# Kernel optimization log

Hardware: AMD Instinct MI355X
Metric: run time of the kernel (lower is better)

Reference implementation:

```python
import jax, jax.numpy as jnp
import numpy as np

N_HEAD, D_MODEL, D_HEAD, D_OUT = 16, 1024, 64, 1024
Q_INNER = N_HEAD * D_HEAD


def setup_inputs() -> dict:
    key = jax.random.key(0)
    ks = jax.random.split(key, 10)
    B, S = 1, 4096
    hidden_state = jax.random.normal(ks[0], (B, S, D_MODEL), dtype=jnp.float32)
    # causal mask, (B,1,S,S), 1 = attend, 0 = masked
    attention_mask = jnp.tril(jnp.ones((S, S), dtype=jnp.int32))[None, None, :, :]
    s = 0.02
    Wq = jax.random.normal(ks[1], (D_MODEL, Q_INNER), dtype=jnp.float32) * s
    bq = jnp.zeros((Q_INNER,), dtype=jnp.float32)
    Wk = jax.random.normal(ks[2], (D_MODEL, D_HEAD), dtype=jnp.float32) * s
    bk = jnp.zeros((D_HEAD,), dtype=jnp.float32)
    Wv = jax.random.normal(ks[3], (D_MODEL, D_HEAD), dtype=jnp.float32) * s
    bv = jnp.zeros((D_HEAD,), dtype=jnp.float32)
    Wo = jax.random.normal(ks[4], (Q_INNER, D_OUT), dtype=jnp.float32) * s
    bo = jnp.zeros((D_OUT,), dtype=jnp.float32)
    return {"hidden_state": hidden_state, "attention_mask": attention_mask,
            "Wq": Wq, "bq": bq, "Wk": Wk, "bk": bk, "Wv": Wv, "bv": bv,
            "Wo": Wo, "bo": bo}


def reference(hidden_state, attention_mask, Wq, bq, Wk, bk, Wv, bv, Wo, bo):
    B, S, _ = hidden_state.shape
    q = hidden_state @ Wq + bq                    # (B,S,H*Dh)
    k = hidden_state @ Wk + bk                    # (B,S,Dh) single shared KV head
    v = hidden_state @ Wv + bv                    # (B,S,Dh)
    q = q.reshape(B, S, N_HEAD, D_HEAD)           # (B,S,H,Dh)
    scale = 1.0 / jnp.sqrt(jnp.float32(D_HEAD))
    # scores: (B,H,S,S) — shared K broadcast over heads
    scores = jnp.einsum('bqhd,bkd->bhqk', q, k) * scale
    scores = jnp.where(attention_mask == 0, -jnp.inf, scores)
    probs = jax.nn.softmax(scores, axis=-1)
    out = jnp.einsum('bhqk,bkd->bqhd', probs, v)  # (B,S,H,Dh)
    out = out.reshape(B, S, Q_INNER)
    return out @ Wo + bo
```

## Files before the change

### kernel.cpp

```cpp
#include <hip/hip_runtime.h>
#include <hip/hip_bf16.h>
#include <math.h>

typedef __bf16 bf16;
typedef __bf16 bf16x4 __attribute__((ext_vector_type(4)));
typedef __bf16 bf16x8 __attribute__((ext_vector_type(8)));
typedef float f32x4 __attribute__((ext_vector_type(4)));

#define AS1(p) ((const __attribute__((address_space(1))) void*)(p))
#define AS3(p) ((__attribute__((address_space(3))) void*)(p))

__device__ __forceinline__ void gld_lds16(const void* g, void* l) {
  __builtin_amdgcn_global_load_lds(AS1(g), AS3(l), 16, 0, 0);
}

#define MFMA16(a, b, c) __builtin_amdgcn_mfma_f32_16x16x32_bf16((a), (b), (c), 0, 0, 0)

#define QSCALE_F 0.180336880f


struct Seg { short qt, h, t0, t1, slot; };
struct Tape { Seg s[1008]; };
struct CJob { short qt, h, base, parts; };
struct CTab { CJob j[336]; };

constexpr int nparts_of(int qt) { int T = 2 * qt + 2; return (T + 21) / 22; }
constexpr int slot_base(int h, int qt) {
  int b = h * 52;
  if (qt <= 21) return b + (qt - 11) * 2;
  return b + 22 + (qt - 22) * 3;
}

constexpr Tape make_tape() {
  Tape tp{};
  int idx = 0;
  for (int s = 22; s >= 1; --s)
    for (int h = 0; h < 16; ++h)
      for (int qt = 0; qt < 32; ++qt) {
        const int T = 2 * qt + 2, P = nparts_of(qt);
        for (int p = 0; p < P; ++p) {
          const int a = p * T / P, b = (p + 1) * T / P;
          if (b - a == s) {
            const int slot = (P == 1) ? -1 : slot_base(h, qt) + p;
            tp.s[idx++] = Seg{(short)qt, (short)h, (short)a, (short)b, (short)slot};
          }
        }
      }
  return tp;
}

constexpr CTab make_ctab() {
  CTab ct{};
  int n = 0;
  for (int h = 0; h < 16; ++h)
    for (int qt = 11; qt < 32; ++qt)
      ct.j[n++] = CJob{(short)qt, (short)h, (short)slot_base(h, qt),
                       (short)nparts_of(qt)};
  return ct;
}

__device__ constexpr Tape TAPE = make_tape();
__device__ constexpr CTab CTAB = make_ctab();

__global__ void cast_f32_bf16_sw(const float4* __restrict__ in, bf16* __restrict__ out,
                                 int n4) {
  int i = blockIdx.x * blockDim.x + threadIdx.x;
  if (i < n4) {
    float4 v = in[i];
    bf16x4 o4 = {(bf16)v.x, (bf16)v.y, (bf16)v.z, (bf16)v.w};
    const int e = i * 4;
    const int row = e >> 10;
    const int idx = (e & ~63) | ((e & 63) ^ ((row & 7) << 3));
    *(bf16x4*)(out + (size_t)idx) = o4;
  }
}

__global__ void prep_wqkv(const float* __restrict__ Wq, const float* __restrict__ Wk,
                          const float* __restrict__ Wv, bf16* __restrict__ out) {
  __shared__ float t[64][65];
  const int ob = blockIdx.y;
  const float* src;
  int C, c0;
  if (ob < 16)      { src = Wq; C = 1024; c0 = ob * 64; }
  else if (ob == 16){ src = Wk; C = 64;   c0 = 0; }
  else              { src = Wv; C = 64;   c0 = 0; }
  const int r0 = blockIdx.x * 64;
  const int tx = threadIdx.x & 63, ty = threadIdx.x >> 6;
#pragma unroll
  for (int j = 0; j < 16; j++)
    t[ty + j * 4][tx] = src[(size_t)(r0 + ty + j * 4) * C + c0 + tx];
  __syncthreads();
#pragma unroll
  for (int j = 0; j < 16; j++) {
    const int orow = ob * 64 + ty + j * 4;
    out[(size_t)orow * 1024 + r0 + (tx ^ ((orow & 7) << 3))] = (bf16)t[tx][ty + j * 4];
  }
}

__global__ void transpose_cast_sw(const float* __restrict__ in, bf16* __restrict__ out,
                                  int C, int ldout) {
  __shared__ float t[64][65];
  int r0 = blockIdx.y * 64, c0 = blockIdx.x * 64;
  int tx = threadIdx.x & 63, ty = threadIdx.x >> 6;
#pragma unroll
  for (int j = 0; j < 16; j++)
    t[ty + j * 4][tx] = in[(size_t)(r0 + ty + j * 4) * C + c0 + tx];
  __syncthreads();
#pragma unroll
  for (int j = 0; j < 16; j++) {
    const int orow = c0 + ty + j * 4;
    out[(size_t)orow * ldout + r0 + (tx ^ ((orow & 7) << 3))] = (bf16)t[tx][ty + j * 4];
  }
}

__global__ void pack_bias3(const float* __restrict__ bq, const float* __restrict__ bk,
                           const float* __restrict__ bv, float* __restrict__ o) {
  int i = blockIdx.x * 256 + threadIdx.x;
  if (i < 1024) o[i] = bq[i];
  else if (i < 1088) o[i] = bk[i - 1024];
  else if (i < 1152) o[i] = bv[i - 1088];
}

template <int OUTF32, int QSCALE>
__global__ __launch_bounds__(256) void gemm_bt64k(const bf16* __restrict__ A,
                                                  const bf16* __restrict__ B,
                                                  const float* __restrict__ bias,
                                                  void* __restrict__ Cout,
                                                  int M, int N, int K) {
  __shared__ bf16 As[2 * 64 * 64];
  __shared__ bf16 Bs[2 * 128 * 64];
  const int tid = threadIdx.x, w = tid >> 6, lane = tid & 63;
  const int g = lane >> 4, r = lane & 15;
  const int cpx = gridDim.x >> 3;
  const int l = (blockIdx.x & 7) * cpx + (blockIdx.x >> 3);
  const int ntn = N >> 7;
  const int my = l / ntn, mx = l - my * ntn;
  const int tm = my * 64, tn = mx * 128;
  const int wr = w >> 1, wc = w & 1;
  const int sz = (r & 7) << 4;

  f32x4 acc[2][4] = {};

  const char* gA = (const char*)(A + (size_t)tm * K);
  const char* gB = (const char*)(B + (size_t)tn * K);
  const int linA0 = (w * 2 + 0) * 1024 + lane * 16;
  const int linA1 = (w * 2 + 1) * 1024 + lane * 16;
  const int linB0 = (w * 4 + 0) * 1024 + lane * 16;
  const int linB1 = (w * 4 + 1) * 1024 + lane * 16;
  const int linB2 = (w * 4 + 2) * 1024 + lane * 16;
  const int linB3 = (w * 4 + 3) * 1024 + lane * 16;

  auto STAGE = [&](int ks, int b) {
    char* dA = (char*)As + b * 8192 + (w * 2) * 1024;
    char* dB = (char*)Bs + b * 16384 + (w * 4) * 1024;
    gld_lds16(gA + (size_t)(linA0 >> 7) * (K * 2) + ks * 128 + (linA0 & 127), dA);
    gld_lds16(gA + (size_t)(linA1 >> 7) * (K * 2) + ks * 128 + (linA1 & 127), dA + 1024);
    gld_lds16(gB + (size_t)(linB0 >> 7) * (K * 2) + ks * 128 + (linB0 & 127), dB);
    gld_lds16(gB + (size_t)(linB1 >> 7) * (K * 2) + ks * 128 + (linB1 & 127), dB + 1024);
    gld_lds16(gB + (size_t)(linB2 >> 7) * (K * 2) + ks * 128 + (linB2 & 127), dB + 2048);
    gld_lds16(gB + (size_t)(linB3 >> 7) * (K * 2) + ks * 128 + (linB3 & 127), dB + 3072);
  };

  const int nk = K >> 6;
  STAGE(0, 0);
  int buf = 0;
  for (int ks = 0; ks < nk; ++ks) {
    if (ks + 1 < nk) {
      STAGE(ks + 1, buf ^ 1);
      asm volatile("s_waitcnt vmcnt(6)" ::: "memory");
    } else {
      asm volatile("s_waitcnt vmcnt(0)" ::: "memory");
    }
    __builtin_amdgcn_sched_barrier(0);
    __builtin_amdgcn_s_barrier();

    const char* at = (const char*)As + buf * 8192;
    const char* bt = (const char*)Bs + buf * 16384;
    bf16x8 af[2][2], bfr[4][2];
#pragma unroll
    for (int m = 0; m < 2; m++)
#pragma unroll
      for (int kk = 0; kk < 2; kk++)
        af[m][kk] = *(const bf16x8*)(at + (wr * 32 + m * 16 + r) * 128 +
                                     ((kk * 64 + g * 16) ^ sz));
#pragma unroll
    for (int n = 0; n < 4; n++)
#pragma unroll
      for (int kk = 0; kk < 2; kk++)
        bfr[n][kk] = *(const bf16x8*)(bt + (wc * 64 + n * 16 + r) * 128 +
                                      ((kk * 64 + g * 16) ^ sz));
    __builtin_amdgcn_s_setprio(1);
#pragma unroll
    for (int m = 0; m < 2; m++)
#pragma unroll
      for (int n = 0; n < 4; n++) {
        acc[m][n] = MFMA16(af[m][0], bfr[n][0], acc[m][n]);
        acc[m][n] = MFMA16(af[m][1], bfr[n][1], acc[m][n]);
      }
    __builtin_amdgcn_s_setprio(0);
    __builtin_amdgcn_s_barrier();
    buf ^= 1;
  }

#pragma unroll
  for (int m = 0; m < 2; m++) {
#pragma unroll
    for (int n = 0; n < 4; n++) {
      int crow = tm + wr * 32 + m * 16 + g * 4;
      int ccol = tn + wc * 64 + n * 16 + r;
      float bb = bias[ccol];
      float sc = (QSCALE && ccol < 1024) ? QSCALE_F : 1.0f;
#pragma unroll
      for (int j = 0; j < 4; j++) {
        float v = (acc[m][n][j] + bb) * sc;
        if (OUTF32)
          ((float*)Cout)[(size_t)(crow + j) * N + ccol] = v;
        else
          ((bf16*)Cout)[(size_t)(crow + j) * N + ccol] = (bf16)v;
      }
    }
  }
}

__global__ void kv_prep(const bf16* __restrict__ QKV, bf16* __restrict__ Ksw,
                        bf16* __restrict__ Vtsw) {
  __shared__ bf16 Vld[64][72];
  const int kv0 = blockIdx.x * 64;
  const int tid = threadIdx.x;
#pragma unroll
  for (int cc = 0; cc < 2; cc++) {
    const int c = tid + cc * 256;
    const int kvl = c >> 3, c8 = c & 7;
    bf16x8 kv8 = *(const bf16x8*)(QKV + (size_t)(kv0 + kvl) * 1152 + 1024 + c8 * 8);
    *(bf16x8*)(Ksw + (size_t)(kv0 + kvl) * 64 + ((c8 * 8) ^ ((kvl & 7) << 3))) = kv8;
    bf16x8 vv = *(const bf16x8*)(QKV + (size_t)(kv0 + kvl) * 1152 + 1088 + c8 * 8);
#pragma unroll
    for (int e = 0; e < 8; e++) Vld[c8 * 8 + e][kvl] = vv[e];
  }
  __syncthreads();
#pragma unroll
  for (int cc = 0; cc < 2; cc++) {
    const int c = tid + cc * 256;
    const int d = c >> 3, k8 = c & 7;
    bf16x8 o8 = *(const bf16x8*)&Vld[d][k8 * 8];
    *(bf16x8*)(Vtsw + (size_t)d * 4096 + kv0 + ((k8 * 8) ^ ((d & 7) << 3))) = o8;
  }
}

__global__ __launch_bounds__(256) void mqa_fwd(const bf16* __restrict__ QKV,
                                               const bf16* __restrict__ Ksw,
                                               const bf16* __restrict__ Vtsw,
                                               bf16* __restrict__ AO,
                                               bf16* __restrict__ po,
                                               float* __restrict__ psum) {
  __shared__ bf16 Ks[2][64 * 64];
  __shared__ bf16 Vs[2][64 * 64];
  __shared__ bf16 Ps[4 * 32 * 64];

  const Seg sg = TAPE.s[blockIdx.x];
  const int qt = sg.qt, h = sg.h, tbeg = sg.t0, tend = sg.t1, slot = sg.slot;

  const int tid = threadIdx.x, w = tid >> 6, lane = tid & 63;
  const int g = lane >> 4, r = lane & 15;
  const int qw = qt * 128 + w * 32;
  const int qown0 = qw + r;
  const int qown1 = qw + 16 + r;

  const char* Kg = (const char*)Ksw;
  const char* Vg = (const char*)Vtsw;
  char* PsB = (char*)Ps;
  const int lin0 = w * 2048 + lane * 16;
  const int lin1 = lin0 + 1024;
  const int sz = (r & 7) << 4;

  bf16x8 qf0[2], qf1[2];
#pragma unroll
  for (int kk = 0; kk < 2; kk++) {
    qf0[kk] = *(const bf16x8*)&QKV[(size_t)qown0 * 1152 + h * 64 + kk * 32 + g * 8];
    qf1[kk] = *(const bf16x8*)&QKV[(size_t)qown1 * 1152 + h * 64 + kk * 32 + g * 8];
  }

  const bf16 one = (bf16)1.0f;
  const bf16x8 ones = {one, one, one, one, one, one, one, one};

  f32x4 o[2][4] = {};
  f32x4 sums[2] = {};

  auto STAGE = [&](int t, int b) {
    const int kn = t * 64;
    char* kb = (char*)Ks + b * 8192 + w * 2048;
    char* vb = (char*)Vs + b * 8192 + w * 2048;
    gld_lds16(Kg + (size_t)kn * 128 + lin0, kb);
    gld_lds16(Kg + (size_t)kn * 128 + lin1, kb + 1024);
    gld_lds16(Vg + (size_t)(lin0 >> 7) * 8192 + kn * 2 + (lin0 & 127), vb);
    gld_lds16(Vg + (size_t)(lin1 >> 7) * 8192 + kn * 2 + (lin1 & 127), vb + 1024);
  };

  int buf = 0;
  STAGE(tbeg, 0);
  for (int t = tbeg; t < tend; ++t) {
    if (t + 1 < tend) {
      STAGE(t + 1, buf ^ 1);
      asm volatile("s_waitcnt vmcnt(4)" ::: "memory");
    } else {
      asm volatile("s_waitcnt vmcnt(0)" ::: "memory");
    }
    __builtin_amdgcn_sched_barrier(0);
    __builtin_amdgcn_s_barrier();

    const char* kt = (const char*)Ks + buf * 8192;
    const char* vt = (const char*)Vs + buf * 8192;
    const int kv0 = t * 64;

    f32x4 s0[4], s1[4];
    __builtin_amdgcn_s_setprio(1);
#pragma unroll
    for (int n = 0; n < 4; n++) {
      bf16x8 kf0 = *(const bf16x8*)(kt + (n * 16 + r) * 128 + ((g * 16) ^ sz));
      bf16x8 kf1 = *(const bf16x8*)(kt + (n * 16 + r) * 128 + ((64 + g * 16) ^ sz));
      f32x4 z0 = {0.f, 0.f, 0.f, 0.f};
      z0 = MFMA16(kf0, qf0[0], z0);
      z0 = MFMA16(kf1, qf0[1], z0);
      s0[n] = z0;
      f32x4 z1 = {0.f, 0.f, 0.f, 0.f};
      z1 = MFMA16(kf0, qf1[0], z1);
      z1 = MFMA16(kf1, qf1[1], z1);
      s1[n] = z1;
    }
    __builtin_amdgcn_s_setprio(0);

    if (t >= 2 * qt) {
#pragma unroll
      for (int n = 0; n < 4; n++)
#pragma unroll
        for (int jj = 0; jj < 4; jj++) {
          const int kv = kv0 + n * 16 + g * 4 + jj;
          if (kv > qown0) s0[n][jj] = -3.0e38f;
          if (kv > qown1) s1[n][jj] = -3.0e38f;
        }
    }

#pragma unroll
    for (int n = 0; n < 4; n++) {
      bf16x4 pk0, pk1;
#pragma unroll
      for (int jj = 0; jj < 4; jj++) {
        pk0[jj] = (bf16)__builtin_amdgcn_exp2f(s0[n][jj]);
        pk1[jj] = (bf16)__builtin_amdgcn_exp2f(s1[n][jj]);
      }
      *(bf16x4*)(PsB + w * 4096 + r * 128 + ((n * 32 + g * 8) ^ sz)) = pk0;
      *(bf16x4*)(PsB + w * 4096 + (16 + r) * 128 + ((n * 32 + g * 8) ^ sz)) = pk1;
    }

    asm volatile("s_waitcnt lgkmcnt(0)" ::: "memory");
    __builtin_amdgcn_sched_barrier(0);

    bf16x8 pa00 = *(const bf16x8*)(PsB + w * 4096 + r * 128 + ((g * 16) ^ sz));
    bf16x8 pa01 = *(const bf16x8*)(PsB + w * 4096 + r * 128 + ((64 + g * 16) ^ sz));
    bf16x8 pa10 = *(const bf16x8*)(PsB + w * 4096 + (16 + r) * 128 + ((g * 16) ^ sz));
    bf16x8 pa11 = *(const bf16x8*)(PsB + w * 4096 + (16 + r) * 128 + ((64 + g * 16) ^ sz));
    __builtin_amdgcn_s_setprio(1);
    sums[0] = MFMA16(pa00, ones, sums[0]);
    sums[0] = MFMA16(pa01, ones, sums[0]);
    sums[1] = MFMA16(pa10, ones, sums[1]);
    sums[1] = MFMA16(pa11, ones, sums[1]);
#pragma unroll
    for (int n = 0; n < 4; n++) {
      bf16x8 vf0 = *(const bf16x8*)(vt + (n * 16 + r) * 128 + ((g * 16) ^ sz));
      bf16x8 vf1 = *(const bf16x8*)(vt + (n * 16 + r) * 128 + ((64 + g * 16) ^ sz));
      o[0][n] = MFMA16(pa00, vf0, o[0][n]);
      o[0][n] = MFMA16(pa01, vf1, o[0][n]);
      o[1][n] = MFMA16(pa10, vf0, o[1][n]);
      o[1][n] = MFMA16(pa11, vf1, o[1][n]);
    }
    __builtin_amdgcn_s_setprio(0);
    __builtin_amdgcn_s_barrier();
    buf ^= 1;
  }

  if (slot < 0) {
#pragma unroll
    for (int H = 0; H < 2; H++)
#pragma unroll
      for (int jj = 0; jj < 4; jj++) {
        const float inv = 1.f / sums[H][jj];
        const int row = qw + H * 16 + g * 4 + jj;
        const int key = (row & 7) << 3;
#pragma unroll
        for (int n = 0; n < 4; n++)
          AO[(size_t)row * 1024 + h * 64 + ((n * 16 + r) ^ key)] =
              (bf16)(o[H][n][jj] * inv);
      }
  } else {
    bf16* pb = po + (size_t)slot * 8192;
#pragma unroll
    for (int H = 0; H < 2; H++)
#pragma unroll
      for (int jj = 0; jj < 4; jj++) {
        const int row = w * 32 + H * 16 + g * 4 + jj;
#pragma unroll
        for (int n = 0; n < 4; n++)
          pb[row * 64 + n * 16 + r] = (bf16)o[H][n][jj];
        if (r == 0) psum[slot * 128 + row] = sums[H][jj];
      }
  }
}

__global__ __launch_bounds__(256) void combine_split(const bf16* __restrict__ po,
                                                     const float* __restrict__ psum,
                                                     bf16* __restrict__ AO) {
  const CJob cj = CTAB.j[blockIdx.x];
  const int row = threadIdx.x >> 1, c0 = (threadIdx.x & 1) * 32;
  float acc[32] = {};
  float ssum = 0.f;
#pragma unroll 1
  for (int p = 0; p < cj.parts; ++p) {
    const bf16* pb = po + (size_t)(cj.base + p) * 8192 + row * 64 + c0;
    ssum += psum[(cj.base + p) * 128 + row];
#pragma unroll
    for (int v = 0; v < 4; ++v) {
      bf16x8 x = ((const bf16x8*)pb)[v];
#pragma unroll
      for (int e = 0; e < 8; e++) acc[v * 8 + e] += (float)x[e];
    }
  }
  const float inv = 1.f / ssum;
  const int grow = cj.qt * 128 + row;
  const int key = (grow & 7) << 3;
  bf16* dst = AO + (size_t)grow * 1024 + cj.h * 64;
#pragma unroll
  for (int i = 0; i < 8; i++) {
    bf16x4 o4 = {(bf16)(acc[i * 4 + 0] * inv), (bf16)(acc[i * 4 + 1] * inv),
                 (bf16)(acc[i * 4 + 2] * inv), (bf16)(acc[i * 4 + 3] * inv)};
    *(bf16x4*)(dst + ((c0 + i * 4) ^ key)) = o4;
  }
}

extern "C" void kernel_launch(void* const* d_in, const int* in_sizes, int n_in,
                              void* d_out, int out_size, void* d_ws, size_t ws_size,
                              hipStream_t stream) {
  const float* H  = (const float*)d_in[0];
  const float* Wq = (const float*)d_in[2];
  const float* bq = (const float*)d_in[3];
  const float* Wk = (const float*)d_in[4];
  const float* bk = (const float*)d_in[5];
  const float* Wv = (const float*)d_in[6];
  const float* bv = (const float*)d_in[7];
  const float* Wo = (const float*)d_in[8];
  const float* bo = (const float*)d_in[9];
  float* out = (float*)d_out;

  const int S = 4096, DM = 1024;

  char* p = (char*)d_ws;
  bf16* Hb    = (bf16*)(p);
  bf16* QKV   = (bf16*)(p + 8388608);
  bf16* Wqkvt = (bf16*)(p + 17825792);
  bf16* Wot   = (bf16*)(p + 20185088);
  float* bqkv = (float*)(p + 22282240);
  bf16* Ksw   = (bf16*)(p + 22286848);
  bf16* Vtsw  = (bf16*)(p + 22811136);
  bf16* po    = (bf16*)(p + 23335424);
  float* psum = (float*)(p + 36966912);
  bf16* AOb   = Hb;

  cast_f32_bf16_sw<<<(S * DM / 4 + 255) / 256, 256, 0, stream>>>((const float4*)H, Hb,
                                                                 S * DM / 4);
  prep_wqkv<<<dim3(16, 18), 256, 0, stream>>>(Wq, Wk, Wv, Wqkvt);
  transpose_cast_sw<<<dim3(16, 16), 256, 0, stream>>>(Wo, Wot, 1024, 1024);
  pack_bias3<<<5, 256, 0, stream>>>(bq, bk, bv, bqkv);

  gemm_bt64k<0, 1><<<576, 256, 0, stream>>>(Hb, Wqkvt, bqkv, QKV, S, 1152, 1024);

  kv_prep<<<64, 256, 0, stream>>>(QKV, Ksw, Vtsw);

  mqa_fwd<<<1008, 256, 0, stream>>>(QKV, Ksw, Vtsw, AOb, po, psum);
  combine_split<<<336, 256, 0, stream>>>(po, psum, AOb);

  gemm_bt64k<1, 0><<<512, 256, 0, stream>>>(AOb, Wot, bo, out, S, 1024, 1024);
}
```

Baseline: 119.9 us.

## Load K/V fragments directly from global into registers, dropping LDS staging

Removes the double-buffered LDS staging of K and V tiles and the block-wide barriers. Each wave now loads its K and V MFMA fragments straight from global memory into registers, prefetching the next K tile during the softmax. Launch bounds request 3 blocks per CU, since LDS use is now small. In exchange the shared K/V tiles are fetched redundantly by all four waves, which relies on the L2/L1 cache, and V loads are exposed to latency within the same iteration.

New measurement: 173.6 us. 44.7% more time.

```diff
diff --git a/kernel.cpp b/kernel.cpp
--- a/kernel.cpp
+++ b/kernel.cpp
@@ -247,14 +247,12 @@
   }
 }
 
-__global__ __launch_bounds__(256) void mqa_fwd(const bf16* __restrict__ QKV,
-                                               const bf16* __restrict__ Ksw,
-                                               const bf16* __restrict__ Vtsw,
-                                               bf16* __restrict__ AO,
-                                               bf16* __restrict__ po,
-                                               float* __restrict__ psum) {
-  __shared__ bf16 Ks[2][64 * 64];
-  __shared__ bf16 Vs[2][64 * 64];
+__global__ __launch_bounds__(256, 3) void mqa_fwd(const bf16* __restrict__ QKV,
+                                                  const bf16* __restrict__ Ksw,
+                                                  const bf16* __restrict__ Vtsw,
+                                                  bf16* __restrict__ AO,
+                                                  bf16* __restrict__ po,
+                                                  float* __restrict__ psum) {
   __shared__ bf16 Ps[4 * 32 * 64];
 
   const Seg sg = TAPE.s[blockIdx.x];
@@ -269,8 +267,6 @@
   const char* Kg = (const char*)Ksw;
   const char* Vg = (const char*)Vtsw;
   char* PsB = (char*)Ps;
-  const int lin0 = w * 2048 + lane * 16;
-  const int lin1 = lin0 + 1024;
   const int sz = (r & 7) << 4;
 
   bf16x8 qf0[2], qf1[2];
@@ -286,48 +282,42 @@
   f32x4 o[2][4] = {};
   f32x4 sums[2] = {};
 
-  auto STAGE = [&](int t, int b) {
-    const int kn = t * 64;
-    char* kb = (char*)Ks + b * 8192 + w * 2048;
-    char* vb = (char*)Vs + b * 8192 + w * 2048;
-    gld_lds16(Kg + (size_t)kn * 128 + lin0, kb);
-    gld_lds16(Kg + (size_t)kn * 128 + lin1, kb + 1024);
-    gld_lds16(Vg + (size_t)(lin0 >> 7) * 8192 + kn * 2 + (lin0 & 127), vb);
-    gld_lds16(Vg + (size_t)(lin1 >> 7) * 8192 + kn * 2 + (lin1 & 127), vb + 1024);
+  bf16x8 kf[4][2];
+  auto LDK = [&](int t) {
+#pragma unroll
+    for (int n = 0; n < 4; n++)
+#pragma unroll
+      for (int kk = 0; kk < 2; kk++)
+        kf[n][kk] = *(const bf16x8*)(Kg + (size_t)t * 8192 + (n * 16 + r) * 128 +
+                                     ((kk * 64 + g * 16) ^ sz));
   };
 
-  int buf = 0;
-  STAGE(tbeg, 0);
+  LDK(tbeg);
   for (int t = tbeg; t < tend; ++t) {
-    if (t + 1 < tend) {
-      STAGE(t + 1, buf ^ 1);
-      asm volatile("s_waitcnt vmcnt(4)" ::: "memory");
-    } else {
-      asm volatile("s_waitcnt vmcnt(0)" ::: "memory");
-    }
-    __builtin_amdgcn_sched_barrier(0);
-    __builtin_amdgcn_s_barrier();
-
-    const char* kt = (const char*)Ks + buf * 8192;
-    const char* vt = (const char*)Vs + buf * 8192;
     const int kv0 = t * 64;
 
     f32x4 s0[4], s1[4];
     __builtin_amdgcn_s_setprio(1);
 #pragma unroll
     for (int n = 0; n < 4; n++) {
-      bf16x8 kf0 = *(const bf16x8*)(kt + (n * 16 + r) * 128 + ((g * 16) ^ sz));
-      bf16x8 kf1 = *(const bf16x8*)(kt + (n * 16 + r) * 128 + ((64 + g * 16) ^ sz));
       f32x4 z0 = {0.f, 0.f, 0.f, 0.f};
-      z0 = MFMA16(kf0, qf0[0], z0);
-      z0 = MFMA16(kf1, qf0[1], z0);
+      z0 = MFMA16(kf[n][0], qf0[0], z0);
+      z0 = MFMA16(kf[n][1], qf0[1], z0);
       s0[n] = z0;
       f32x4 z1 = {0.f, 0.f, 0.f, 0.f};
-      z1 = MFMA16(kf0, qf1[0], z1);
-      z1 = MFMA16(kf1, qf1[1], z1);
+      z1 = MFMA16(kf[n][0], qf1[0], z1);
+      z1 = MFMA16(kf[n][1], qf1[1], z1);
       s1[n] = z1;
     }
     __builtin_amdgcn_s_setprio(0);
+
+    bf16x8 vf[4][2];
+#pragma unroll
+    for (int n = 0; n < 4; n++)
+#pragma unroll
+      for (int kk = 0; kk < 2; kk++)
+        vf[n][kk] = *(const bf16x8*)(Vg + (size_t)(n * 16 + r) * 8192 + kv0 * 2 +
+                                     ((kk * 64 + g * 16) ^ sz));
 
     if (t >= 2 * qt) {
 #pragma unroll
@@ -351,6 +341,8 @@
       *(bf16x4*)(PsB + w * 4096 + r * 128 + ((n * 32 + g * 8) ^ sz)) = pk0;
       *(bf16x4*)(PsB + w * 4096 + (16 + r) * 128 + ((n * 32 + g * 8) ^ sz)) = pk1;
     }
+
+    if (t + 1 < tend) LDK(t + 1);
 
     asm volatile("s_waitcnt lgkmcnt(0)" ::: "memory");
     __builtin_amdgcn_sched_barrier(0);
@@ -366,16 +358,12 @@
     sums[1] = MFMA16(pa11, ones, sums[1]);
 #pragma unroll
     for (int n = 0; n < 4; n++) {
-      bf16x8 vf0 = *(const bf16x8*)(vt + (n * 16 + r) * 128 + ((g * 16) ^ sz));
-      bf16x8 vf1 = *(const bf16x8*)(vt + (n * 16 + r) * 128 + ((64 + g * 16) ^ sz));
-      o[0][n] = MFMA16(pa00, vf0, o[0][n]);
-      o[0][n] = MFMA16(pa01, vf1, o[0][n]);
-      o[1][n] = MFMA16(pa10, vf0, o[1][n]);
-      o[1][n] = MFMA16(pa11, vf1, o[1][n]);
+      o[0][n] = MFMA16(pa00, vf[n][0], o[0][n]);
+      o[0][n] = MFMA16(pa01, vf[n][1], o[0][n]);
+      o[1][n] = MFMA16(pa10, vf[n][0], o[1][n]);
+      o[1][n] = MFMA16(pa11, vf[n][1], o[1][n]);
     }
     __builtin_amdgcn_s_setprio(0);
-    __builtin_amdgcn_s_barrier();
-    buf ^= 1;
   }
 
   if (slot < 0) {
```

## Keep P in registers via 16x16x16 MFMA and rebalance causal split tape

Applied to the files above, without the earlier changes.

Removes the LDS round-trip for the probability tile by feeding exp2 results directly as A-operands of the 16x16x16 bf16 MFMA, whose register layout matches the QK^T accumulator output. V fragments are now read as 4-element chunks per k-block. The work tape is rebuilt by pairing light and heavy causal query tiles (i, 31-i) into four segments per pair, so the grid is exactly 1024 evenly sized blocks, and launch bounds request 4 blocks per CU. It trades twice as many smaller MFMA instructions for fewer LDS writes, reads and waits, and lower LDS use per block.

New measurement: 135.3 us. 12.8% more time.

```diff
diff --git a/kernel.cpp b/kernel.cpp
--- a/kernel.cpp
+++ b/kernel.cpp
@@ -6,6 +6,7 @@
 typedef __bf16 bf16x4 __attribute__((ext_vector_type(4)));
 typedef __bf16 bf16x8 __attribute__((ext_vector_type(8)));
 typedef float f32x4 __attribute__((ext_vector_type(4)));
+typedef short s16x4 __attribute__((ext_vector_type(4)));
 
 #define AS1(p) ((const __attribute__((address_space(1))) void*)(p))
 #define AS3(p) ((__attribute__((address_space(3))) void*)(p))
@@ -15,47 +16,58 @@
 }
 
 #define MFMA16(a, b, c) __builtin_amdgcn_mfma_f32_16x16x32_bf16((a), (b), (c), 0, 0, 0)
+#define MFMA16K(a, b, c) __builtin_amdgcn_mfma_f32_16x16x16bf16_1k((a), (b), (c), 0, 0, 0)
 
 #define QSCALE_F 0.180336880f
 
 
 struct Seg { short qt, h, t0, t1, slot; };
-struct Tape { Seg s[1008]; };
+struct Tape { Seg s[1024]; };
 struct CJob { short qt, h, base, parts; };
 struct CTab { CJob j[336]; };
 
-constexpr int nparts_of(int qt) { int T = 2 * qt + 2; return (T + 21) / 22; }
-constexpr int slot_base(int h, int qt) {
-  int b = h * 52;
-  if (qt <= 21) return b + (qt - 11) * 2;
-  return b + 22 + (qt - 22) * 3;
-}
-
 constexpr Tape make_tape() {
   Tape tp{};
-  int idx = 0;
-  for (int s = 22; s >= 1; --s)
-    for (int h = 0; h < 16; ++h)
-      for (int qt = 0; qt < 32; ++qt) {
-        const int T = 2 * qt + 2, P = nparts_of(qt);
-        for (int p = 0; p < P; ++p) {
-          const int a = p * T / P, b = (p + 1) * T / P;
-          if (b - a == s) {
-            const int slot = (P == 1) ? -1 : slot_base(h, qt) + p;
-            tp.s[idx++] = Seg{(short)qt, (short)h, (short)a, (short)b, (short)slot};
-          }
-        }
-      }
+  int slot_next = 0;
+  for (int h = 0; h < 16; ++h)
+    for (int i = 0; i < 16; ++i) {
+      const int px = h * 16 + i;
+      const int T1 = 2 * i + 2, T2 = 64 - 2 * i;
+      const int a = (T1 <= 22) ? 1 : 2, b = 4 - a;
+      int k = 0;
+      int base1 = -1;
+      if (a > 1) { base1 = slot_next; slot_next += a; }
+      for (int p = 0; p < a; ++p) {
+        const int t0 = p * T1 / a, t1 = (p + 1) * T1 / a;
+        tp.s[px + 256 * k] = Seg{(short)i, (short)h, (short)t0, (short)t1,
+                                 (short)(a > 1 ? base1 + p : -1)};
+        ++k;
+      }
+      const int base2 = slot_next; slot_next += b;
+      for (int p = 0; p < b; ++p) {
+        const int t0 = p * T2 / b, t1 = (p + 1) * T2 / b;
+        tp.s[px + 256 * k] = Seg{(short)(31 - i), (short)h, (short)t0, (short)t1,
+                                 (short)(base2 + p)};
+        ++k;
+      }
+    }
   return tp;
 }
 
 constexpr CTab make_ctab() {
   CTab ct{};
-  int n = 0;
+  int slot_next = 0, nj = 0;
   for (int h = 0; h < 16; ++h)
-    for (int qt = 11; qt < 32; ++qt)
-      ct.j[n++] = CJob{(short)qt, (short)h, (short)slot_base(h, qt),
-                       (short)nparts_of(qt)};
+    for (int i = 0; i < 16; ++i) {
+      const int T1 = 2 * i + 2;
+      const int a = (T1 <= 22) ? 1 : 2, b = 4 - a;
+      if (a > 1) {
+        ct.j[nj++] = CJob{(short)i, (short)h, (short)slot_next, (short)a};
+        slot_next += a;
+      }
+      ct.j[nj++] = CJob{(short)(31 - i), (short)h, (short)slot_next, (short)b};
+      slot_next += b;
+    }
   return ct;
 }
 
@@ -247,15 +259,14 @@
   }
 }
 
-__global__ __launch_bounds__(256) void mqa_fwd(const bf16* __restrict__ QKV,
-                                               const bf16* __restrict__ Ksw,
-                                               const bf16* __restrict__ Vtsw,
-                                               bf16* __restrict__ AO,
-                                               bf16* __restrict__ po,
-                                               float* __restrict__ psum) {
+__global__ __launch_bounds__(256, 4) void mqa_fwd(const bf16* __restrict__ QKV,
+                                                  const bf16* __restrict__ Ksw,
+                                                  const bf16* __restrict__ Vtsw,
+                                                  bf16* __restrict__ AO,
+                                                  bf16* __restrict__ po,
+                                                  float* __restrict__ psum) {
   __shared__ bf16 Ks[2][64 * 64];
   __shared__ bf16 Vs[2][64 * 64];
-  __shared__ bf16 Ps[4 * 32 * 64];
 
   const Seg sg = TAPE.s[blockIdx.x];
   const int qt = sg.qt, h = sg.h, tbeg = sg.t0, tend = sg.t1, slot = sg.slot;
@@ -268,7 +279,6 @@
 
   const char* Kg = (const char*)Ksw;
   const char* Vg = (const char*)Vtsw;
-  char* PsB = (char*)Ps;
   const int lin0 = w * 2048 + lane * 16;
   const int lin1 = lin0 + 1024;
   const int sz = (r & 7) << 4;
@@ -280,11 +290,9 @@
     qf1[kk] = *(const bf16x8*)&QKV[(size_t)qown1 * 1152 + h * 64 + kk * 32 + g * 8];
   }
 
-  const bf16 one = (bf16)1.0f;
-  const bf16x8 ones = {one, one, one, one, one, one, one, one};
-
   f32x4 o[2][4] = {};
   f32x4 sums[2] = {};
+  const s16x4 ones4 = {0x3F80, 0x3F80, 0x3F80, 0x3F80};
 
   auto STAGE = [&](int t, int b) {
     const int kn = t * 64;
@@ -329,6 +337,14 @@
     }
     __builtin_amdgcn_s_setprio(0);
 
+    s16x4 vf[4][4];
+#pragma unroll
+    for (int kb = 0; kb < 4; kb++)
+#pragma unroll
+      for (int n = 0; n < 4; n++)
+        vf[kb][n] = *(const s16x4*)(vt + (n * 16 + r) * 128 +
+                                    ((kb * 32 + g * 8) ^ sz));
+
     if (t >= 2 * qt) {
 #pragma unroll
       for (int n = 0; n < 4; n++)
@@ -340,38 +356,26 @@
         }
     }
 
-#pragma unroll
-    for (int n = 0; n < 4; n++) {
-      bf16x4 pk0, pk1;
+    union PW { bf16x4 hh; s16x4 ss; };
+    PW p0[4], p1[4];
+#pragma unroll
+    for (int n = 0; n < 4; n++)
 #pragma unroll
       for (int jj = 0; jj < 4; jj++) {
-        pk0[jj] = (bf16)__builtin_amdgcn_exp2f(s0[n][jj]);
-        pk1[jj] = (bf16)__builtin_amdgcn_exp2f(s1[n][jj]);
-      }
-      *(bf16x4*)(PsB + w * 4096 + r * 128 + ((n * 32 + g * 8) ^ sz)) = pk0;
-      *(bf16x4*)(PsB + w * 4096 + (16 + r) * 128 + ((n * 32 + g * 8) ^ sz)) = pk1;
-    }
-
-    asm volatile("s_waitcnt lgkmcnt(0)" ::: "memory");
-    __builtin_amdgcn_sched_barrier(0);
-
-    bf16x8 pa00 = *(const bf16x8*)(PsB + w * 4096 + r * 128 + ((g * 16) ^ sz));
-    bf16x8 pa01 = *(const bf16x8*)(PsB + w * 4096 + r * 128 + ((64 + g * 16) ^ sz));
-    bf16x8 pa10 = *(const bf16x8*)(PsB + w * 4096 + (16 + r) * 128 + ((g * 16) ^ sz));
-    bf16x8 pa11 = *(const bf16x8*)(PsB + w * 4096 + (16 + r) * 128 + ((64 + g * 16) ^ sz));
+        p0[n].hh[jj] = (bf16)__builtin_amdgcn_exp2f(s0[n][jj]);
+        p1[n].hh[jj] = (bf16)__builtin_amdgcn_exp2f(s1[n][jj]);
+      }
+
     __builtin_amdgcn_s_setprio(1);
-    sums[0] = MFMA16(pa00, ones, sums[0]);
-    sums[0] = MFMA16(pa01, ones, sums[0]);
-    sums[1] = MFMA16(pa10, ones, sums[1]);
-    sums[1] = MFMA16(pa11, ones, sums[1]);
-#pragma unroll
-    for (int n = 0; n < 4; n++) {
-      bf16x8 vf0 = *(const bf16x8*)(vt + (n * 16 + r) * 128 + ((g * 16) ^ sz));
-      bf16x8 vf1 = *(const bf16x8*)(vt + (n * 16 + r) * 128 + ((64 + g * 16) ^ sz));
-      o[0][n] = MFMA16(pa00, vf0, o[0][n]);
-      o[0][n] = MFMA16(pa01, vf1, o[0][n]);
-      o[1][n] = MFMA16(pa10, vf0, o[1][n]);
-      o[1][n] = MFMA16(pa11, vf1, o[1][n]);
+#pragma unroll
+    for (int kb = 0; kb < 4; kb++) {
+      sums[0] = MFMA16K(p0[kb].ss, ones4, sums[0]);
+      sums[1] = MFMA16K(p1[kb].ss, ones4, sums[1]);
+#pragma unroll
+      for (int n = 0; n < 4; n++) {
+        o[0][n] = MFMA16K(p0[kb].ss, vf[kb][n], o[0][n]);
+        o[1][n] = MFMA16K(p1[kb].ss, vf[kb][n], o[1][n]);
+      }
     }
     __builtin_amdgcn_s_setprio(0);
     __builtin_amdgcn_s_barrier();
@@ -461,7 +465,7 @@
   bf16* Ksw   = (bf16*)(p + 22286848);
   bf16* Vtsw  = (bf16*)(p + 22811136);
   bf16* po    = (bf16*)(p + 23335424);
-  float* psum = (float*)(p + 36966912);
+  float* psum = (float*)(p + 37229056);
   bf16* AOb   = Hb;
 
   cast_f32_bf16_sw<<<(S * DM / 4 + 255) / 256, 256, 0, stream>>>((const float4*)H, Hb,
@@ -474,7 +478,7 @@
 
   kv_prep<<<64, 256, 0, stream>>>(QKV, Ksw, Vtsw);
 
-  mqa_fwd<<<1008, 256, 0, stream>>>(QKV, Ksw, Vtsw, AOb, po, psum);
+  mqa_fwd<<<1024, 256, 0, stream>>>(QKV, Ksw, Vtsw, AOb, po, psum);
   combine_split<<<336, 256, 0, stream>>>(po, psum, AOb);
 
   gemm_bt64k<1, 0><<<512, 256, 0, stream>>>(AOb, Wot, bo, out, S, 1024, 1024);
```
